# Kernel optimization log

Measured on AMD Instinct MI355X. Metric: run time of the kernel, lower is better.

Reference implementation:

```python
import jax, jax.numpy as jnp
import numpy as np

K_TOP = 4       # top-k experts per token (init arg K)
ALPHA = 1.702   # sigmoid-GLU slope
LIMIT = 7.0     # clamp limit


def setup_inputs() -> dict:
    key = jax.random.key(0)
    ks = jax.random.split(key, 4)
    B, S, H, E, inter = 2, 2048, 1024, 16, 1024
    return {
        "hidden_states": jax.random.normal(ks[0], (B, S, H), dtype=jnp.float32),
        "router_weight": jax.random.normal(ks[1], (E, H), dtype=jnp.float32) * 0.02,
        "router_bias": jnp.zeros((E,), dtype=jnp.float32),
        "gate_up_proj": jax.random.normal(ks[2], (E, H, 2 * inter), dtype=jnp.float32) * 0.02,
        "gate_up_bias": jnp.zeros((E, 2 * inter), dtype=jnp.float32),
        "down_proj": jax.random.normal(ks[3], (E, inter, H), dtype=jnp.float32) * 0.02,
        "down_bias": jnp.zeros((E, H), dtype=jnp.float32),
    }


def reference(hidden_states, router_weight, router_bias, gate_up_proj,
              gate_up_bias, down_proj, down_bias):
    B, S, H = hidden_states.shape
    E, inter, _ = down_proj.shape
    # Router: softmax over experts, top-k selection.
    logits = jnp.einsum('bsh,eh->bse', hidden_states, router_weight) + router_bias
    scores = jax.nn.softmax(logits, axis=-1)                 # (B,S,E)
    topk_w, topk_i = jax.lax.top_k(scores, K_TOP)            # (B,S,K)
    # Dense per-expert GLU MLP (single-device dispatch == identity: every
    # expert sees every token, as in the module's dense einsum path).
    gu = jnp.einsum('bsh,ehn->bsen', hidden_states, gate_up_proj) + gate_up_bias  # (B,S,E,2*inter)
    gate = jnp.minimum(gu[..., :inter], LIMIT)
    up = jnp.clip(gu[..., inter:], -LIMIT, LIMIT)
    glu = gate * jax.nn.sigmoid(gate * ALPHA)
    activated = (up + 1.0) * glu                             # (B,S,E,inter)
    down = jnp.einsum('bsek,ekh->bseh', activated, down_proj) + down_bias  # (B,S,E,H)
    # Combine: gather each token's top-k expert outputs, weighted sum.
    sel = jnp.take_along_axis(down, topk_i[..., None], axis=2)  # (B,S,K,H)
    out = jnp.sum(sel * topk_w[..., None], axis=2)              # (B,S,H)
    return out
```

## Files before the change

### kernel.cpp

```cpp
#include <hip/hip_runtime.h>
#include <stdint.h>

typedef __bf16 bf16;
typedef __bf16 bf16x4 __attribute__((ext_vector_type(4)));
typedef __bf16 bf16x8 __attribute__((ext_vector_type(8)));
typedef float  f32x4  __attribute__((ext_vector_type(4)));

#define TOKENS 4096
#define HDIM   1024
#define NEXP   16
#define KTOP   4
#define NPAIR  (TOKENS*KTOP)

__device__ __forceinline__ void gload16(const void* g, void* l) {
  __builtin_amdgcn_global_load_lds(
      (const __attribute__((address_space(1))) unsigned int*)g,
      (__attribute__((address_space(3))) unsigned int*)l, 16, 0, 0);
}


__global__ __launch_bounds__(256) void conv_hidden(const float* __restrict__ in,
                                                   bf16* __restrict__ out) {
  int i = blockIdx.x * 256 + threadIdx.x;
  float4 v = ((const float4*)in)[i];
  bf16x4 o = { (bf16)v.x, (bf16)v.y, (bf16)v.z, (bf16)v.w };
  ((bf16x4*)out)[i] = o;
}

template<int NCOLS, bool ILV>
__global__ __launch_bounds__(256) void conv_w(const float* __restrict__ src,
                                              bf16* __restrict__ dst) {
  __shared__ float tile[32][65];
  const int e = blockIdx.z;
  const int n0 = blockIdx.x * 64, k0 = blockIdx.y * 32;
  const float* S = src + (size_t)e * 1024 * NCOLS;
  bf16* D = dst + (size_t)e * NCOLS * 1024;
  int tx = threadIdx.x & 63, ty = threadIdx.x >> 6;
#pragma unroll
  for (int j = 0; j < 8; ++j)
    tile[ty*8 + j][tx] = S[(size_t)(k0 + ty*8 + j) * NCOLS + n0 + tx];
  __syncthreads();
  int kx = threadIdx.x & 31, nyb = threadIdx.x >> 5;
#pragma unroll
  for (int j = 0; j < 8; ++j) {
    int nl = nyb*8 + j;
    int n2 = n0 + nl;
    int rp;
    if (ILV) {
      int a = (n2 < 1024) ? n2 : (n2 - 1024);
      rp = (a >> 5) * 64 + (a & 31) + ((n2 < 1024) ? 0 : 32);
    } else {
      rp = n2;
    }
    D[(size_t)rp * 1024 + k0 + kx] = (bf16)tile[kx][nl];
  }
}


__global__ __launch_bounds__(256) void router_k(const float* __restrict__ hs,
                                                const float* __restrict__ rw,
                                                const float* __restrict__ rb,
                                                int* __restrict__ topk_e,
                                                float* __restrict__ topk_w) {
  const int t = blockIdx.x;
  const float* h = hs + (size_t)t * HDIM;
  const int e = threadIdx.x >> 4, l16 = threadIdx.x & 15;
  const float* w = rw + (size_t)e * HDIM;
  float p = 0.f;
#pragma unroll
  for (int j = 0; j < 16; ++j) {
    int k = l16 * 4 + j * 64;
    float4 hv = *(const float4*)(h + k);
    float4 wv = *(const float4*)(w + k);
    p += hv.x*wv.x + hv.y*wv.y + hv.z*wv.z + hv.w*wv.w;
  }
#pragma unroll
  for (int m = 8; m >= 1; m >>= 1) p += __shfl_xor(p, m, 16);
  __shared__ float logits[NEXP];
  if (l16 == 0) logits[e] = p + rb[e];
  __syncthreads();
  if (threadIdx.x == 0) {
    float mx = logits[0];
    for (int i = 1; i < NEXP; ++i) mx = fmaxf(mx, logits[i]);
    float sc[NEXP]; float s = 0.f;
    for (int i = 0; i < NEXP; ++i) { sc[i] = expf(logits[i] - mx); s += sc[i]; }
    float inv = 1.f / s;
    unsigned used = 0;
    for (int k = 0; k < KTOP; ++k) {
      int bi = -1; float bv = -1e30f;
      for (int i = 0; i < NEXP; ++i)
        if (!((used >> i) & 1) && sc[i] > bv) { bv = sc[i]; bi = i; }
      used |= 1u << bi;
      topk_e[t*KTOP + k] = bi;
      topk_w[t*KTOP + k] = bv * inv;
    }
  }
}


__global__ __launch_bounds__(1024) void assign_all(const int* __restrict__ topk_e,
                                                   int* __restrict__ offsets,
                                                   int* __restrict__ token_pos,
                                                   int* __restrict__ pos2tok) {
  __shared__ int cnt[NEXP];
  __shared__ int off[NEXP + 1];
  __shared__ int cur[NEXP];
  const int tid = threadIdx.x;
  if (tid < NEXP) { cnt[tid] = 0; cur[tid] = 0; }
  __syncthreads();
  int myE[16];
#pragma unroll
  for (int j = 0; j < 16; ++j) {
    int s = tid + j * 1024;
    myE[j] = topk_e[s];
    atomicAdd(&cnt[myE[j]], 1);
  }
  __syncthreads();
  if (tid == 0) {
    int a = 0;
    for (int e2 = 0; e2 < NEXP; ++e2) { off[e2] = a; a += cnt[e2]; }
    off[NEXP] = a;
  }
  __syncthreads();
  if (tid < NEXP + 1) offsets[tid] = off[tid];
#pragma unroll
  for (int j = 0; j < 16; ++j) {
    int s = tid + j * 1024;
    int e2 = myE[j];
    int pos = off[e2] + atomicAdd(&cur[e2], 1);
    token_pos[s] = pos;
    pos2tok[pos] = s >> 2;
  }
}


template<bool GATHER, bool ACT>
__global__ __launch_bounds__(256)
void gemm_moe(const bf16* __restrict__ A, const bf16* __restrict__ Bw,
              const int* __restrict__ pos2tok, const int* __restrict__ offsets,
              const float* __restrict__ gu_bias, bf16* __restrict__ Cout, int NB) {
  __shared__ bf16 sm[2 * 128 * 64];
  const int e  = blockIdx.y >> 5;
  const int rt = blockIdx.y & 31;
  const int start = offsets[e] + rt * 128;
  const int end   = offsets[e + 1];
  if (start >= end) return;
  int rows_valid = end - start; if (rows_valid > 128) rows_valid = 128;
  const int tN  = blockIdx.x;
  const int tid = threadIdx.x, wid = tid >> 6, lane = tid & 63;

  const bf16* Asrc[4];
#pragma unroll
  for (int i = 0; i < 4; ++i) {
    int r = i*32 + wid*8 + (lane >> 3);
    long row;
    if (GATHER) {
      int g = start + r; if (g > NPAIR - 1) g = NPAIR - 1;
      row = pos2tok[g];
    } else {
      row = start + r;
    }
    Asrc[i] = A + row * 1024 + (lane & 7) * 8;
  }
  const bf16* Bsrc[4];
#pragma unroll
  for (int i = 0; i < 4; ++i) {
    int r = tN * 128 + i*32 + wid*8 + (lane >> 3);
    Bsrc[i] = Bw + ((long)e * NB + r) * 1024 + (lane & 7) * 8;
  }

  f32x4 zero = {0.f, 0.f, 0.f, 0.f};
  f32x4 acc[4][4];
#pragma unroll
  for (int m = 0; m < 4; ++m)
#pragma unroll
    for (int n = 0; n < 4; ++n) acc[m][n] = zero;

  const int wr = wid >> 1, wc = wid & 1;
  const bf16* Al = sm + ((wr*64 + (lane & 15)) * 64) + (lane >> 4) * 8;
  const bf16* Bl = sm + 128*64 + ((wc*64 + (lane & 15)) * 64) + (lane >> 4) * 8;

  for (int k0 = 0; k0 < 1024; k0 += 64) {
#pragma unroll
    for (int i = 0; i < 4; ++i) {
      gload16(Asrc[i] + k0, (char*)sm + (i*32 + wid*8) * 128);
      gload16(Bsrc[i] + k0, (char*)sm + 16384 + (i*32 + wid*8) * 128);
    }
    __syncthreads();
#pragma unroll
    for (int kk = 0; kk < 2; ++kk) {
      bf16x8 af[4], bfr[4];
#pragma unroll
      for (int m = 0; m < 4; ++m) af[m]  = *(const bf16x8*)(Al + m*16*64 + kk*32);
#pragma unroll
      for (int n = 0; n < 4; ++n) bfr[n] = *(const bf16x8*)(Bl + n*16*64 + kk*32);
#pragma unroll
      for (int m = 0; m < 4; ++m)
#pragma unroll
        for (int n = 0; n < 4; ++n)
          acc[m][n] = __builtin_amdgcn_mfma_f32_16x16x32_bf16(af[m], bfr[n], acc[m][n], 0, 0, 0);
    }
    __syncthreads();
  }

  const int c = lane & 15;
  const int rbase = (lane >> 4) * 4;
  if constexpr (ACT) {
#pragma unroll
    for (int p = 0; p < 2; ++p) {
      int a = tN*64 + wc*32 + p*16 + c;
      float bg = gu_bias[e*2048 + a];
      float bu = gu_bias[e*2048 + 1024 + a];
#pragma unroll
      for (int m = 0; m < 4; ++m)
#pragma unroll
        for (int r = 0; r < 4; ++r) {
          int rl = wr*64 + m*16 + rbase + r;
          if (rl < rows_valid) {
            float g = acc[m][p][r] + bg;       g = fminf(g, 7.f);
            float u = acc[m][p + 2][r] + bu;   u = fminf(fmaxf(u, -7.f), 7.f);
            float sig = 1.f / (1.f + __expf(-1.702f * g));
            float av = (u + 1.f) * (g * sig);
            Cout[(long)(start + rl) * 1024 + a] = (bf16)av;
          }
        }
    }
  } else {
#pragma unroll
    for (int n = 0; n < 4; ++n) {
      int col = tN*128 + wc*64 + n*16 + c;
#pragma unroll
      for (int m = 0; m < 4; ++m)
#pragma unroll
        for (int r = 0; r < 4; ++r) {
          int rl = wr*64 + m*16 + rbase + r;
          if (rl < rows_valid)
            Cout[(long)(start + rl) * 1024 + col] = (bf16)acc[m][n][r];
        }
    }
  }
}


__global__ __launch_bounds__(256) void combine_k(const bf16* __restrict__ pair,
                                                 const float* __restrict__ dn_bias,
                                                 const int* __restrict__ token_pos,
                                                 const int* __restrict__ topk_e,
                                                 const float* __restrict__ topk_w,
                                                 float* __restrict__ out) {
  const int t = blockIdx.x;
  const int cidx = threadIdx.x * 4;
  float4 o = {0.f, 0.f, 0.f, 0.f};
#pragma unroll
  for (int k = 0; k < KTOP; ++k) {
    int pos = token_pos[t*KTOP + k];
    int e   = topk_e[t*KTOP + k];
    float w = topk_w[t*KTOP + k];
    bf16x4 v = *(const bf16x4*)(pair + (long)pos * 1024 + cidx);
    float4 b = *(const float4*)(dn_bias + (size_t)e * 1024 + cidx);
    o.x += w * ((float)v[0] + b.x);
    o.y += w * ((float)v[1] + b.y);
    o.z += w * ((float)v[2] + b.z);
    o.w += w * ((float)v[3] + b.w);
  }
  *(float4*)(out + (long)t * 1024 + cidx) = o;
}


extern "C" void kernel_launch(void* const* d_in, const int* in_sizes, int n_in,
                              void* d_out, int out_size, void* d_ws, size_t ws_size,
                              hipStream_t stream) {
  const float* hs  = (const float*)d_in[0];
  const float* rw  = (const float*)d_in[1];
  const float* rb  = (const float*)d_in[2];
  const float* guw = (const float*)d_in[3];
  const float* gub = (const float*)d_in[4];
  const float* dnw = (const float*)d_in[5];
  const float* dnb = (const float*)d_in[6];
  float* out = (float*)d_out;

  char* w = (char*)d_ws;
  int*   offsets   = (int*)(w + 256);
  int*   topk_e    = (int*)(w + 1024);
  float* topk_w    = (float*)(w + 1024 + 65536);
  int*   token_pos = (int*)(w + 1024 + 2*65536);
  int*   pos2tok   = (int*)(w + 1024 + 3*65536);
  char*  big = w + 1024 + 4*65536;
  bf16* gu_wt = (bf16*)(big);
  bf16* dn_wt = (bf16*)(big + 67108864);
  bf16* hbf   = (bf16*)(big + 100663296);
  bf16* act   = (bf16*)(big + 109051904);
  bf16* pair  = (bf16*)(big + 142868480);

  conv_hidden<<<4096, 256, 0, stream>>>(hs, hbf);
  conv_w<2048, true ><<<dim3(32, 32, 16), 256, 0, stream>>>(guw, gu_wt);
  conv_w<1024, false><<<dim3(16, 32, 16), 256, 0, stream>>>(dnw, dn_wt);
  router_k<<<TOKENS, 256, 0, stream>>>(hs, rw, rb, topk_e, topk_w);
  assign_all<<<1, 1024, 0, stream>>>(topk_e, offsets, token_pos, pos2tok);
  gemm_moe<true,  true ><<<dim3(16, 512), 256, 0, stream>>>(hbf, gu_wt, pos2tok, offsets, gub, act, 2048);
  gemm_moe<false, false><<<dim3(8, 512), 256, 0, stream>>>(act, dn_wt, pos2tok, offsets, nullptr, pair, 1024);
  combine_k<<<TOKENS, 256, 0, stream>>>(pair, dnb, token_pos, topk_e, topk_w, out);
}
```

Baseline: 525.1 us.

## Double-buffer GEMM LDS tiles and widen weight conversion tiles with bf16 staging

The MoE GEMM now uses two LDS buffers and issues the global-to-LDS loads for the next K-slice before computing the current one, so memory latency overlaps with MFMA work. The weight transpose/convert kernel stages bf16 values in a 64x64 tile and writes paired bf16 stores, halving its grid. Doubling LDS per block to 64KB may reduce occupancy.

```diff
diff --git a/kernel.cpp b/kernel.cpp
--- a/kernel.cpp
+++ b/kernel.cpp
@@ -2,6 +2,7 @@
 #include <stdint.h>
 
 typedef __bf16 bf16;
+typedef __bf16 bf16x2 __attribute__((ext_vector_type(2)));
 typedef __bf16 bf16x4 __attribute__((ext_vector_type(4)));
 typedef __bf16 bf16x8 __attribute__((ext_vector_type(8)));
 typedef float  f32x4  __attribute__((ext_vector_type(4)));
@@ -30,20 +31,22 @@
 template<int NCOLS, bool ILV>
 __global__ __launch_bounds__(256) void conv_w(const float* __restrict__ src,
                                               bf16* __restrict__ dst) {
-  __shared__ float tile[32][65];
+  __shared__ bf16 tile[64][66];
   const int e = blockIdx.z;
-  const int n0 = blockIdx.x * 64, k0 = blockIdx.y * 32;
+  const int n0 = blockIdx.x * 64, k0 = blockIdx.y * 64;
   const float* S = src + (size_t)e * 1024 * NCOLS;
   bf16* D = dst + (size_t)e * NCOLS * 1024;
-  int tx = threadIdx.x & 63, ty = threadIdx.x >> 6;
-#pragma unroll
-  for (int j = 0; j < 8; ++j)
-    tile[ty*8 + j][tx] = S[(size_t)(k0 + ty*8 + j) * NCOLS + n0 + tx];
-  __syncthreads();
-  int kx = threadIdx.x & 31, nyb = threadIdx.x >> 5;
+  const int tx = threadIdx.x & 63, ty = threadIdx.x >> 6;
+#pragma unroll
+  for (int j = 0; j < 16; ++j) {
+    int kr = ty * 16 + j;
+    tile[tx][kr] = (bf16)S[(size_t)(k0 + kr) * NCOLS + n0 + tx];
+  }
+  __syncthreads();
+  const int kh = threadIdx.x & 31, nr = threadIdx.x >> 5;
 #pragma unroll
   for (int j = 0; j < 8; ++j) {
-    int nl = nyb*8 + j;
+    int nl = j * 8 + nr;
     int n2 = n0 + nl;
     int rp;
     if (ILV) {
@@ -52,7 +55,8 @@
     } else {
       rp = n2;
     }
-    D[(size_t)rp * 1024 + k0 + kx] = (bf16)tile[kx][nl];
+    bf16x2 v = *(const bf16x2*)&tile[nl][kh * 2];
+    *(bf16x2*)&D[(size_t)rp * 1024 + k0 + kh * 2] = v;
   }
 }
 
@@ -139,7 +143,7 @@
 void gemm_moe(const bf16* __restrict__ A, const bf16* __restrict__ Bw,
               const int* __restrict__ pos2tok, const int* __restrict__ offsets,
               const float* __restrict__ gu_bias, bf16* __restrict__ Cout, int NB) {
-  __shared__ bf16 sm[2 * 128 * 64];
+  __shared__ bf16 sm[2][2 * 128 * 64];
   const int e  = blockIdx.y >> 5;
   const int rt = blockIdx.y & 31;
   const int start = offsets[e] + rt * 128;
@@ -177,23 +181,37 @@
     for (int n = 0; n < 4; ++n) acc[m][n] = zero;
 
   const int wr = wid >> 1, wc = wid & 1;
-  const bf16* Al = sm + ((wr*64 + (lane & 15)) * 64) + (lane >> 4) * 8;
-  const bf16* Bl = sm + 128*64 + ((wc*64 + (lane & 15)) * 64) + (lane >> 4) * 8;
-
-  for (int k0 = 0; k0 < 1024; k0 += 64) {
-#pragma unroll
-    for (int i = 0; i < 4; ++i) {
-      gload16(Asrc[i] + k0, (char*)sm + (i*32 + wid*8) * 128);
-      gload16(Bsrc[i] + k0, (char*)sm + 16384 + (i*32 + wid*8) * 128);
-    }
-    __syncthreads();
+  const int aoff = (wr*64 + (lane & 15)) * 64 + (lane >> 4) * 8;
+  const int boff = 8192 + (wc*64 + (lane & 15)) * 64 + (lane >> 4) * 8;
+  const int stg  = (wid*8 + (lane >> 3)) * 128;
+
+#pragma unroll
+  for (int i = 0; i < 4; ++i) {
+    gload16(Asrc[i], (char*)sm + i*32*128 + stg);
+    gload16(Bsrc[i], (char*)sm + 16384 + i*32*128 + stg);
+  }
+  __syncthreads();
+
+#pragma unroll
+  for (int t = 0; t < 16; ++t) {
+    const int cur = t & 1;
+    if (t < 15) {
+      const int k0 = (t + 1) * 64;
+      const int nb = (cur ^ 1) * 32768;
+#pragma unroll
+      for (int i = 0; i < 4; ++i) {
+        gload16(Asrc[i] + k0, (char*)sm + nb + i*32*128 + stg);
+        gload16(Bsrc[i] + k0, (char*)sm + nb + 16384 + i*32*128 + stg);
+      }
+    }
+    const bf16* base = sm[cur];
 #pragma unroll
     for (int kk = 0; kk < 2; ++kk) {
       bf16x8 af[4], bfr[4];
 #pragma unroll
-      for (int m = 0; m < 4; ++m) af[m]  = *(const bf16x8*)(Al + m*16*64 + kk*32);
-#pragma unroll
-      for (int n = 0; n < 4; ++n) bfr[n] = *(const bf16x8*)(Bl + n*16*64 + kk*32);
+      for (int m = 0; m < 4; ++m) af[m]  = *(const bf16x8*)(base + aoff + m*16*64 + kk*32);
+#pragma unroll
+      for (int n = 0; n < 4; ++n) bfr[n] = *(const bf16x8*)(base + boff + n*16*64 + kk*32);
 #pragma unroll
       for (int m = 0; m < 4; ++m)
 #pragma unroll
@@ -293,8 +311,8 @@
   bf16* pair  = (bf16*)(big + 142868480);
 
   conv_hidden<<<4096, 256, 0, stream>>>(hs, hbf);
-  conv_w<2048, true ><<<dim3(32, 32, 16), 256, 0, stream>>>(guw, gu_wt);
-  conv_w<1024, false><<<dim3(16, 32, 16), 256, 0, stream>>>(dnw, dn_wt);
+  conv_w<2048, true ><<<dim3(32, 16, 16), 256, 0, stream>>>(guw, gu_wt);
+  conv_w<1024, false><<<dim3(16, 16, 16), 256, 0, stream>>>(dnw, dn_wt);
   router_k<<<TOKENS, 256, 0, stream>>>(hs, rw, rb, topk_e, topk_w);
   assign_all<<<1, 1024, 0, stream>>>(topk_e, offsets, token_pos, pos2tok);
   gemm_moe<true,  true ><<<dim3(16, 512), 256, 0, stream>>>(hbf, gu_wt, pos2tok, offsets, gub, act, 2048);
```

After: 487.6 us. 7.1% less time.
